# Optimization experiments

Hardware: AMD Instinct MI355X
Metric: run time of the kernel (lower is better)

The kernel has to match this reference:

```python
import math
import jax, jax.numpy as jnp
import numpy as np

IN_DIM, OUT_DIM, NUM_BASIS = 128, 64, 8
EPS = 1e-5

def _periods():
    # periods[i,j,g] = i*(out_dim*num_basis) + j*num_basis + g + 2
    i = jnp.arange(OUT_DIM)[:, None, None]
    j = jnp.arange(OUT_DIM)[None, :, None]
    g = jnp.arange(NUM_BASIS)[None, None, :]
    return (i * (OUT_DIM * NUM_BASIS) + j * NUM_BASIS + g + 2).astype(jnp.float32)

def setup_inputs() -> dict:
    key = jax.random.key(0)
    k1, k2, k3, k4 = jax.random.split(key, 4)
    x = jax.random.normal(k1, (2, 512, IN_DIM), dtype=jnp.float32)
    positions = jnp.arange(512, dtype=jnp.int32)
    M = jax.random.uniform(k2, (OUT_DIM, IN_DIM), minval=-0.5, maxval=0.5, dtype=jnp.float32)
    P = jax.random.uniform(k3, (OUT_DIM, OUT_DIM, NUM_BASIS), minval=-0.1, maxval=0.1, dtype=jnp.float32)
    gamma = jnp.ones((OUT_DIM,), dtype=jnp.float32)
    beta = jnp.zeros((OUT_DIM,), dtype=jnp.float32)
    Wres = jax.random.uniform(k4, (OUT_DIM, IN_DIM), minval=-0.1, maxval=0.1, dtype=jnp.float32)
    return {"x": x, "positions": positions, "M": M, "P": P, "gamma": gamma, "beta": beta, "Wres": Wres}

def reference(x, positions, M, P, gamma, beta, Wres):
    # x: (b, s, in), M: (out, in)
    x_trans = jnp.einsum('bsc,oc->bso', x, M)
    mu = jnp.mean(x_trans, axis=-1, keepdims=True)
    var = jnp.mean(jnp.square(x_trans - mu), axis=-1, keepdims=True)
    x_trans = (x_trans - mu) * jax.lax.rsqrt(var + EPS) * gamma + beta
    # phi[s,i,j,g] = cos(2*pi*k_s / periods[i,j,g])
    k = positions.astype(jnp.float32)[:, None, None, None]
    phi = jnp.cos(2.0 * math.pi * k / _periods())  # (s, out, out, nb)
    # Nk[b,s,i] = sum_{j,g} P[i,j,g] * x_trans[b,s,j] * phi[s,i,j,g]
    W = jnp.einsum('sijg,ijg->sij', phi, P)  # (s, out, out)
    Nk = jnp.einsum('bsj,sij->bsi', x_trans, W)
    residual = jnp.einsum('bsc,oc->bso', x, Wres)  # separate residual proj (in!=out)
    return Nk + residual
```

## Files before the change

kernel.cpp:

```cpp
#include <hip/hip_runtime.h>
#include <hip/hip_bf16.h>

#define IN_DIM    128
#define OUT_DIM   64
#define NUM_BASIS 8
#define SEQ       512
#define BATCH     2
#define EPS       1e-5f

__global__ __launch_bounds__(256) void fused_layerts_kernel(
    const float* __restrict__ x,
    const float* __restrict__ M,
    const float* __restrict__ Wres,
    const float* __restrict__ gamma,
    const float* __restrict__ beta,
    const float* __restrict__ P,
    const int*   __restrict__ positions,
    float* __restrict__ out)
{
    const int s   = blockIdx.x;
    const int tid = threadIdx.x;

    __shared__ float xs[BATCH][IN_DIM];
    __shared__ float xts[BATCH][OUT_DIM];
    __shared__ float rs[BATCH][OUT_DIM];
    __shared__ float part[4][BATCH][OUT_DIM];

    {
        const int b = tid >> 7;
        const int c = tid & 127;
        xs[b][c] = x[((size_t)b * SEQ + s) * IN_DIM + c];
    }
    const float k = (float)positions[s];
    __syncthreads();

    if (tid < BATCH * OUT_DIM) {
        const int b = tid >> 6;
        const int o = tid & 63;

        const float4* x4 = reinterpret_cast<const float4*>(xs[b]);
        const float4* m4 = reinterpret_cast<const float4*>(M    + (size_t)o * IN_DIM);
        const float4* w4 = reinterpret_cast<const float4*>(Wres + (size_t)o * IN_DIM);

        float macc = 0.f, racc = 0.f;
#pragma unroll
        for (int c = 0; c < IN_DIM / 4; ++c) {
            float4 xv = x4[c];
            float4 mv = m4[c];
            float4 wv = w4[c];
            macc += xv.x * mv.x + xv.y * mv.y + xv.z * mv.z + xv.w * mv.w;
            racc += xv.x * wv.x + xv.y * wv.y + xv.z * wv.z + xv.w * wv.w;
        }

        float ssum = macc;
#pragma unroll
        for (int off = 32; off > 0; off >>= 1) ssum += __shfl_xor(ssum, off);
        const float mu = ssum * (1.0f / OUT_DIM);

        const float d = macc - mu;
        float v = d * d;
#pragma unroll
        for (int off = 32; off > 0; off >>= 1) v += __shfl_xor(v, off);
        const float var = v * (1.0f / OUT_DIM);

        xts[b][o] = d * rsqrtf(var + EPS) * gamma[o] + beta[o];
        rs[b][o]  = racc;
    }
    __syncthreads();

    const int i   = tid & 63;
    const int grp = tid >> 6;

    float nk0 = 0.f, nk1 = 0.f;

#pragma unroll 4
    for (int jj = 0; jj < 16; ++jj) {
        const int j    = grp * 16 + jj;
        const int base = (i * OUT_DIM + j) * NUM_BASIS;
        const float4* Pp = reinterpret_cast<const float4*>(P + base);
        const float4 p0 = Pp[0];
        const float4 p1 = Pp[1];
        const float basef = (float)(base + 2);

        const float pv[8] = {p0.x, p0.y, p0.z, p0.w, p1.x, p1.y, p1.z, p1.w};
        float w = 0.f;
#pragma unroll
        for (int g = 0; g < NUM_BASIS; ++g) {
            const float period = basef + (float)g;
            const float inv    = __builtin_amdgcn_rcpf(period);
            float t = k * inv;
            t = __builtin_amdgcn_fractf(t);
            w += pv[g] * __builtin_amdgcn_cosf(t);
        }
        nk0 += xts[0][j] * w;
        nk1 += xts[1][j] * w;
    }

    part[grp][0][i] = nk0;
    part[grp][1][i] = nk1;
    __syncthreads();

    if (tid < BATCH * OUT_DIM) {
        const int b  = tid >> 6;
        const int ii = tid & 63;
        const float sum = part[0][b][ii] + part[1][b][ii] +
                          part[2][b][ii] + part[3][b][ii];
        const size_t idx = ((size_t)b * SEQ + s) * OUT_DIM + ii;
        out[idx] = sum + rs[b][ii];
    }
}

extern "C" void kernel_launch(void* const* d_in, const int* in_sizes, int n_in,
                              void* d_out, int out_size, void* d_ws, size_t ws_size,
                              hipStream_t stream)
{
    const float* x         = (const float*)d_in[0];
    const int*   positions = (const int*)d_in[1];
    const float* M         = (const float*)d_in[2];
    const float* P         = (const float*)d_in[3];
    const float* gamma     = (const float*)d_in[4];
    const float* beta      = (const float*)d_in[5];
    const float* Wres      = (const float*)d_in[6];
    float* out = (float*)d_out;

    hipLaunchKernelGGL(fused_layerts_kernel, dim3(SEQ), dim3(256), 0, stream,
                       x, M, Wres, gamma, beta, P, positions, out);
}
```

Before: 21.30 us.

## Process two sequence positions per block to reuse P loads and reciprocals

Each block now handles two sequence positions with 512 threads. The P coefficients and the reciprocal of each period are computed once and reused for both positions' cosine sums. The input projection is split across two halves of the input dimension, with an extra shared-memory reduction step. This halves the grid to 256 blocks and raises register and shared-memory use per block, which may lower occupancy and leaves fewer blocks than before to cover the GPU's compute units.

```diff
diff --git a/kernel.cpp b/kernel.cpp
--- a/kernel.cpp
+++ b/kernel.cpp
@@ -7,8 +7,9 @@
 #define SEQ       512
 #define BATCH     2
 #define EPS       1e-5f
+#define SX        2
 
-__global__ __launch_bounds__(256) void fused_layerts_kernel(
+__global__ __launch_bounds__(512) void fused_layerts_kernel(
     const float* __restrict__ x,
     const float* __restrict__ M,
     const float* __restrict__ Wres,
@@ -18,39 +19,60 @@
     const int*   __restrict__ positions,
     float* __restrict__ out)
 {
-    const int s   = blockIdx.x;
+    const int s0  = blockIdx.x * SX;
     const int tid = threadIdx.x;
 
-    __shared__ float xs[BATCH][IN_DIM];
-    __shared__ float xts[BATCH][OUT_DIM];
-    __shared__ float rs[BATCH][OUT_DIM];
-    __shared__ float part[4][BATCH][OUT_DIM];
+    __shared__ float xs [SX][BATCH][IN_DIM];
+    __shared__ float xts[SX][BATCH][OUT_DIM];
+    __shared__ float rs [SX][BATCH][OUT_DIM];
+    __shared__ float pm [2][SX * BATCH][OUT_DIM];
+    __shared__ float pr [2][SX * BATCH][OUT_DIM];
+    __shared__ float part[8][SX][BATCH][OUT_DIM];
 
     {
-        const int b = tid >> 7;
-        const int c = tid & 127;
-        xs[b][c] = x[((size_t)b * SEQ + s) * IN_DIM + c];
+        const int row = tid >> 7;
+        const int c   = tid & 127;
+        const int b   = row & 1;
+        const int sl  = row >> 1;
+        xs[sl][b][c] = x[((size_t)b * SEQ + (s0 + sl)) * IN_DIM + c];
     }
-    const float k = (float)positions[s];
+    const float k0 = (float)positions[s0];
+    const float k1 = (float)positions[s0 + 1];
     __syncthreads();
 
-    if (tid < BATCH * OUT_DIM) {
-        const int b = tid >> 6;
-        const int o = tid & 63;
+    {
+        const int o    = tid & 63;
+        const int r    = (tid >> 6) & 3;
+        const int half = tid >> 8;
+        const int b    = r & 1;
+        const int sl   = r >> 1;
 
-        const float4* x4 = reinterpret_cast<const float4*>(xs[b]);
-        const float4* m4 = reinterpret_cast<const float4*>(M    + (size_t)o * IN_DIM);
-        const float4* w4 = reinterpret_cast<const float4*>(Wres + (size_t)o * IN_DIM);
+        const float4* x4 = reinterpret_cast<const float4*>(&xs[sl][b][half * 64]);
+        const float4* m4 = reinterpret_cast<const float4*>(M    + (size_t)o * IN_DIM + half * 64);
+        const float4* w4 = reinterpret_cast<const float4*>(Wres + (size_t)o * IN_DIM + half * 64);
 
         float macc = 0.f, racc = 0.f;
 #pragma unroll
-        for (int c = 0; c < IN_DIM / 4; ++c) {
+        for (int c = 0; c < 16; ++c) {
             float4 xv = x4[c];
             float4 mv = m4[c];
             float4 wv = w4[c];
             macc += xv.x * mv.x + xv.y * mv.y + xv.z * mv.z + xv.w * mv.w;
             racc += xv.x * wv.x + xv.y * wv.y + xv.z * wv.z + xv.w * wv.w;
         }
+        pm[half][r][o] = macc;
+        pr[half][r][o] = racc;
+    }
+    __syncthreads();
+
+    if (tid < SX * BATCH * OUT_DIM) {
+        const int o  = tid & 63;
+        const int r  = tid >> 6;
+        const int b  = r & 1;
+        const int sl = r >> 1;
+
+        const float macc = pm[0][r][o] + pm[1][r][o];
+        const float racc = pr[0][r][o] + pr[1][r][o];
 
         float ssum = macc;
 #pragma unroll
@@ -63,19 +85,19 @@
         for (int off = 32; off > 0; off >>= 1) v += __shfl_xor(v, off);
         const float var = v * (1.0f / OUT_DIM);
 
-        xts[b][o] = d * rsqrtf(var + EPS) * gamma[o] + beta[o];
-        rs[b][o]  = racc;
+        xts[sl][b][o] = d * rsqrtf(var + EPS) * gamma[o] + beta[o];
+        rs [sl][b][o] = racc;
     }
     __syncthreads();
 
     const int i   = tid & 63;
     const int grp = tid >> 6;
 
-    float nk0 = 0.f, nk1 = 0.f;
+    float nk00 = 0.f, nk01 = 0.f, nk10 = 0.f, nk11 = 0.f;
 
-#pragma unroll 4
-    for (int jj = 0; jj < 16; ++jj) {
-        const int j    = grp * 16 + jj;
+#pragma unroll
+    for (int jj = 0; jj < 8; ++jj) {
+        const int j    = grp * 8 + jj;
         const int base = (i * OUT_DIM + j) * NUM_BASIS;
         const float4* Pp = reinterpret_cast<const float4*>(P + base);
         const float4 p0 = Pp[0];
@@ -83,30 +105,40 @@
         const float basef = (float)(base + 2);
 
         const float pv[8] = {p0.x, p0.y, p0.z, p0.w, p1.x, p1.y, p1.z, p1.w};
-        float w = 0.f;
+        float w0 = 0.f, w1 = 0.f;
 #pragma unroll
         for (int g = 0; g < NUM_BASIS; ++g) {
             const float period = basef + (float)g;
-            const float inv    = __builtin_amdgcn_rcpf(period);
-            float t = k * inv;
-            t = __builtin_amdgcn_fractf(t);
-            w += pv[g] * __builtin_amdgcn_cosf(t);
+            const float inv = __builtin_amdgcn_rcpf(period);
+            float t0 = __builtin_amdgcn_fractf(k0 * inv);
+            float t1 = __builtin_amdgcn_fractf(k1 * inv);
+            w0 += pv[g] * __builtin_amdgcn_cosf(t0);
+            w1 += pv[g] * __builtin_amdgcn_cosf(t1);
         }
-        nk0 += xts[0][j] * w;
-        nk1 += xts[1][j] * w;
+        nk00 += xts[0][0][j] * w0;
+        nk01 += xts[0][1][j] * w0;
+        nk10 += xts[1][0][j] * w1;
+        nk11 += xts[1][1][j] * w1;
     }
 
-    part[grp][0][i] = nk0;
-    part[grp][1][i] = nk1;
+    part[grp][0][0][i] = nk00;
+    part[grp][0][1][i] = nk01;
+    part[grp][1][0][i] = nk10;
+    part[grp][1][1][i] = nk11;
     __syncthreads();
 
-    if (tid < BATCH * OUT_DIM) {
-        const int b  = tid >> 6;
-        const int ii = tid & 63;
-        const float sum = part[0][b][ii] + part[1][b][ii] +
-                          part[2][b][ii] + part[3][b][ii];
-        const size_t idx = ((size_t)b * SEQ + s) * OUT_DIM + ii;
-        out[idx] = sum + rs[b][ii];
+    if (tid < SX * BATCH * OUT_DIM) {
+        const int o  = tid & 63;
+        const int r  = tid >> 6;
+        const int b  = r & 1;
+        const int sl = r >> 1;
+
+        float sum = 0.f;
+#pragma unroll
+        for (int gg = 0; gg < 8; ++gg) sum += part[gg][sl][b][o];
+
+        const size_t idx = ((size_t)b * SEQ + (s0 + sl)) * OUT_DIM + o;
+        out[idx] = sum + rs[sl][b][o];
     }
 }
 
@@ -123,6 +155,6 @@
     const float* Wres      = (const float*)d_in[6];
     float* out = (float*)d_out;
 
-    hipLaunchKernelGGL(fused_layerts_kernel, dim3(SEQ), dim3(256), 0, stream,
+    hipLaunchKernelGGL(fused_layerts_kernel, dim3(SEQ / SX), dim3(512), 0, stream,
                        x, M, Wres, gamma, beta, P, positions, out);
 }
```

New measurement: 18.48 us. 13.3% less time.
